# Kernel tuning notes

Measured on AMD Instinct MI355X. Metric: run time of the kernel, lower is better.

## Reference

```python
import jax, jax.numpy as jnp
import numpy as np
import math

B, S, D_MODEL, H = 2, 2048, 2048, 16
HD = D_MODEL // H  # head_dim = 128


def setup_inputs() -> dict:
    key = jax.random.key(0)
    ks = jax.random.split(key, 10)
    x = jax.random.normal(ks[0], (B, S, D_MODEL), dtype=jnp.float32)
    # RoPE tables: interleaved-pair layout matching rotate_half (adjacent dims form pairs)
    inv_freq = 1.0 / (10000.0 ** (jnp.arange(0, HD, 2, dtype=jnp.float32) / HD))  # [HD/2]
    angles = jnp.arange(S, dtype=jnp.float32)[:, None] * inv_freq[None, :]        # [S, HD/2]
    angles = jnp.repeat(angles, 2, axis=-1)                                       # [S, HD]
    cos, sin = jnp.cos(angles), jnp.sin(angles)
    # causal mask (1 = keep), broadcastable to [B,H,S,S]
    attn_mask = jnp.tril(jnp.ones((S, S), dtype=bool))[None, None]
    scale = 1.0 / math.sqrt(D_MODEL)
    Wq = jax.random.normal(ks[1], (D_MODEL, D_MODEL), dtype=jnp.float32) * scale
    Wk = jax.random.normal(ks[2], (D_MODEL, D_MODEL), dtype=jnp.float32) * scale
    Wv = jax.random.normal(ks[3], (D_MODEL, D_MODEL), dtype=jnp.float32) * scale
    Wo = jax.random.normal(ks[4], (D_MODEL, D_MODEL), dtype=jnp.float32) * scale
    bq = jnp.zeros((D_MODEL,), jnp.float32)
    bk = jnp.zeros((D_MODEL,), jnp.float32)
    bv = jnp.zeros((D_MODEL,), jnp.float32)
    bo = jnp.zeros((D_MODEL,), jnp.float32)
    return {"x": x, "cos": cos, "sin": sin, "attn_mask": attn_mask,
            "Wq": Wq, "bq": bq, "Wk": Wk, "bk": bk, "Wv": Wv, "bv": bv, "Wo": Wo, "bo": bo}


def _rotate_half(x):
    # pairs adjacent dims: (x0,x1) -> (-x1,x0)
    xr = x.reshape(*x.shape[:-1], -1, 2)
    x1, x2 = xr[..., 0], xr[..., 1]
    return jnp.stack([-x2, x1], axis=-1).reshape(x.shape)


def reference(x, cos, sin, attn_mask, Wq, bq, Wk, bk, Wv, bv, Wo, bo):
    b, s, _ = x.shape
    q = (x @ Wq.T + bq).reshape(b, s, H, HD).transpose(0, 2, 1, 3)  # [B,H,S,HD]
    k = (x @ Wk.T + bk).reshape(b, s, H, HD).transpose(0, 2, 1, 3)
    v = (x @ Wv.T + bv).reshape(b, s, H, HD).transpose(0, 2, 1, 3)
    c = cos[None, None]  # [1,1,S,HD]
    sn = sin[None, None]
    q = q * c + _rotate_half(q) * sn
    k = k * c + _rotate_half(k) * sn
    scores = jnp.einsum('bhqd,bhkd->bhqk', q, k) / math.sqrt(HD)  # [B,H,S,S]
    scores = jnp.where(attn_mask, scores, -jnp.inf)
    attn = jax.nn.softmax(scores, axis=-1)
    out = jnp.einsum('bhqk,bhkd->bhqd', attn, v)  # [B,H,S,HD]
    out = out.transpose(0, 2, 1, 3).reshape(b, s, H * HD)
    return out @ Wo.T + bo
```

## Files before the change

kernel.cpp:

```cpp
#include <hip/hip_runtime.h>
#include <math.h>

typedef __attribute__((ext_vector_type(8))) __bf16 bf16x8;
typedef __attribute__((ext_vector_type(4))) float f32x4;
typedef __attribute__((ext_vector_type(4))) unsigned short us4;
typedef unsigned short u16;
typedef unsigned int u32;

#define DEVI static __device__ __forceinline__

DEVI u16 f2bf(float f) {
  union { float f; unsigned u; } v; v.f = f;
  unsigned r = v.u + 0x7fffu + ((v.u >> 16) & 1u);
  return (u16)(r >> 16);
}

DEVI void async16(const void* g, void* l) {
  __builtin_amdgcn_global_load_lds((const __attribute__((address_space(1))) void*)g,
                                   (__attribute__((address_space(3))) void*)l, 16, 0, 0);
}

DEVI u32 pkbf(float lo, float hi) {
  u32 r;
  asm("v_cvt_pk_bf16_f32 %0, %1, %2" : "=v"(r) : "v"(lo), "v"(hi));
  return r;
}

__global__ __launch_bounds__(256)
void cast_all(const float* __restrict__ x,
              const float* __restrict__ wq, const float* __restrict__ wk,
              const float* __restrict__ wv, const float* __restrict__ wo,
              u16* __restrict__ xb, u16* __restrict__ wqb, u16* __restrict__ wkb,
              u16* __restrict__ wvb, u16* __restrict__ wob)
{
  const int NX = 4096 * 2048, NW = 2048 * 2048;
  int i = (blockIdx.x * 256 + threadIdx.x) * 4;
  const float* src; u16* dst; int off;
  if (i < NX)               { src = x;  dst = xb;  off = i; }
  else if (i < NX + NW)     { src = wq; dst = wqb; off = i - NX; }
  else if (i < NX + 2 * NW) { src = wk; dst = wkb; off = i - NX - NW; }
  else if (i < NX + 3 * NW) { src = wv; dst = wvb; off = i - NX - 2 * NW; }
  else                      { src = wo; dst = wob; off = i - NX - 3 * NW; }
  float4 v = *(const float4*)(src + off);
  us4 o = { f2bf(v.x), f2bf(v.y), f2bf(v.z), f2bf(v.w) };
  *(us4*)(dst + off) = o;
}

template<int MODE>
__global__ __launch_bounds__(256, 3)
void gemm_bt(const u16* __restrict__ A, const u16* __restrict__ B,
             const float* __restrict__ bias,
             const float* __restrict__ cosT, const float* __restrict__ sinT,
             void* __restrict__ outp)
{
  __shared__ __align__(16) u16 As[8192];
  __shared__ __align__(16) u16 Bs[8192];
  const int t = threadIdx.x, w = t >> 6, lane = t & 63;
  const int lrow = lane & 15, lk8 = (lane >> 4) * 8;
  const int brow = blockIdx.y * 128, bcol = blockIdx.x * 128;
  const int wr = (w >> 1) * 64, wc = (w & 1) * 64;

  u32 sA[4], sB[4];
#pragma unroll
  for (int r = 0; r < 4; ++r) {
    const int q = (r * 256 + t) * 16;
    const int row = q >> 7;
    const int cb = (q ^ ((row & 7) << 4)) & 127;
    sA[r] = (u32)((brow + row) * 2048 + (cb >> 1));
    sB[r] = (u32)((bcol + row) * 2048 + (cb >> 1));
  }

  int offA[4][2], offB[4][2];
#pragma unroll
  for (int m = 0; m < 4; ++m)
#pragma unroll
    for (int kk = 0; kk < 2; ++kk) {
      int row = wr + m * 16 + lrow;
      offA[m][kk] = (row * 128 + (kk * 32 + lk8) * 2) ^ ((row & 7) << 4);
      row = wc + m * 16 + lrow;
      offB[m][kk] = (row * 128 + (kk * 32 + lk8) * 2) ^ ((row & 7) << 4);
    }

  f32x4 acc[4][4] = {};

  for (int k0 = 0; k0 < 2048; k0 += 64) {
#pragma unroll
    for (int r = 0; r < 4; ++r) {
      async16(A + sA[r] + k0, (char*)As + (r * 256 + t) * 16);
      async16(B + sB[r] + k0, (char*)Bs + (r * 256 + t) * 16);
    }
    __syncthreads();
#pragma unroll
    for (int kk = 0; kk < 2; ++kk) {
      bf16x8 a[4], b[4];
#pragma unroll
      for (int m = 0; m < 4; ++m) a[m] = *(const bf16x8*)((char*)As + offA[m][kk]);
#pragma unroll
      for (int n = 0; n < 4; ++n) b[n] = *(const bf16x8*)((char*)Bs + offB[n][kk]);
#pragma unroll
      for (int m = 0; m < 4; ++m)
#pragma unroll
        for (int n = 0; n < 4; ++n)
          acc[m][n] = __builtin_amdgcn_mfma_f32_16x16x32_bf16(a[m], b[n], acc[m][n], 0, 0, 0);
    }
    __syncthreads();
  }

#pragma unroll
  for (int mi = 0; mi < 4; ++mi) {
#pragma unroll
    for (int ni = 0; ni < 4; ++ni) {
      f32x4 v = acc[mi][ni];
      const int row0 = brow + wr + mi * 16 + (lane >> 4) * 4;
      const int col = bcol + wc + ni * 16 + lrow;
      if constexpr (MODE == 3) {
        float* O = (float*)outp;
        const float bv = bias[col];
#pragma unroll
        for (int r = 0; r < 4; ++r)
          O[(size_t)(row0 + r) * 2048 + col] = v[r] + bv;
      } else if constexpr (MODE == 0 || MODE == 1) {
        u16* O = (u16*)outp;
        const float bv = bias[col];
        const int h = col >> 7, d = col & 127;
        const float sgn = (d & 1) ? 1.f : -1.f;
        const float QSCL = 0.08838834764831845f * 1.44269504088896340f;
#pragma unroll
        for (int r = 0; r < 4; ++r) {
          const int row = row0 + r, bb = row >> 11, s = row & 2047;
          float q = v[r] + bv;
          float p = __shfl_xor(q, 1);
          float o = q * cosT[s * 128 + d] + sgn * p * sinT[s * 128 + d];
          if constexpr (MODE == 0) o *= QSCL;
          u16* base = O + ((size_t)(bb * 16 + h) * 2048 + s) * 128;
          if constexpr (MODE == 0) {
            base[d] = f2bf(o);
          } else {
            *(u16*)((char*)base + (((unsigned)(d << 1)) ^ (unsigned)((s & 7) << 4))) = f2bf(o);
          }
        }
      } else {
        u16* O = (u16*)outp;
        const float bv = bias[col];
        const int h = col >> 7, d = col & 127;
        const int bb = row0 >> 11, s = row0 & 2047;
        us4 ov;
#pragma unroll
        for (int r = 0; r < 4; ++r) ov[r] = f2bf(v[r] + bv);
        const int l = s & 63;
        const int kt = l >> 4, g2 = (l >> 2) & 3;
        const int c = ((kt >> 1) << 5) + (g2 << 3) + ((kt & 1) << 2);
        u16* base = O + ((size_t)(bb * 16 + h) * 128 + d) * 2048 + (s & ~63);
        *(us4*)((char*)base + ((unsigned)(c << 1) ^ (unsigned)((d & 7) << 4))) = ov;
      }
    }
  }
}

__global__ __launch_bounds__(256, 2)
void attn_fwd(const u16* __restrict__ Q, const u16* __restrict__ K,
              const u16* __restrict__ Vt, u16* __restrict__ AO)
{
  __shared__ __align__(16) u16 Ks[2][64 * 128];
  __shared__ __align__(16) u16 Vs[2][128 * 64];
  const int t = threadIdx.x, w = t >> 6, lane = t & 63;
  const int lrow = lane & 15, g = lane >> 4, lk8 = g * 8;
  const int id = blockIdx.x;
  const int bh = (id & 7) | (((id >> 3) & 3) << 3);
  const int pr = id >> 5;
  const u16* Qg = Q + (size_t)bh * 2048 * 128;
  const u16* Kg = K + (size_t)bh * 2048 * 128;
  const u16* Vg = Vt + (size_t)bh * 128 * 2048;
  const int bb = bh >> 4, h = bh & 15;

  for (int half = 0; half < 2; ++half) {
    const int qt = half ? (31 - pr) : pr;
    const int q0 = qt * 64, qw = q0 + w * 16;
    const int nkv = qt + 1;
    const int qg = qw + lrow;

    bf16x8 qf[4];
#pragma unroll
    for (int c = 0; c < 4; ++c)
      qf[c] = *(const bf16x8*)(Qg + (size_t)(qw + lrow) * 128 + lk8 + c * 32);

    f32x4 acc_o[8] = {};
    float m = -1e30f, lsum = 0.f;

    auto stage = [&](int i, int b) {
#pragma unroll
      for (int r = 0; r < 4; ++r) {
        int e = (r * 256 + t) * 8;
        async16(Kg + (size_t)i * 8192 + e, &Ks[b][r * 2048 + w * 512]);
        async16(Vg + (size_t)(e >> 6) * 2048 + i * 64 + (e & 63), &Vs[b][r * 2048 + w * 512]);
      }
    };

    stage(0, 0);
    for (int i = 0; i < nkv; ++i) {
      const int cur = i & 1;
      const bool pfch = (i + 1) < nkv;
      if (pfch) stage(i + 1, cur ^ 1);
      if (pfch) asm volatile("s_waitcnt vmcnt(8)" ::: "memory");
      else      asm volatile("s_waitcnt vmcnt(0)" ::: "memory");
      __builtin_amdgcn_s_barrier();
      __builtin_amdgcn_sched_barrier(0);

      f32x4 sc[4];
      __builtin_amdgcn_s_setprio(1);
#pragma unroll
      for (int kt = 0; kt < 4; ++kt) {
        f32x4 s = {};
        const int krow = kt * 16 + lrow;
        const char* kbase = (const char*)(&Ks[cur][krow * 128]);
        const unsigned sw = (unsigned)((krow & 7) << 4);
#pragma unroll
        for (int c = 0; c < 4; ++c) {
          bf16x8 kf = *(const bf16x8*)(kbase + ((unsigned)((lk8 + c * 32) << 1) ^ sw));
          s = __builtin_amdgcn_mfma_f32_16x16x32_bf16(kf, qf[c], s, 0, 0, 0);
        }
        sc[kt] = s;
      }
      __builtin_amdgcn_s_setprio(0);

      float p[4][4];
      const bool lastblk = (i == qt);
      if (lastblk) {
#pragma unroll
        for (int kt = 0; kt < 4; ++kt)
#pragma unroll
          for (int r = 0; r < 4; ++r) {
            int kg = i * 64 + kt * 16 + g * 4 + r;
            p[kt][r] = (kg > qg) ? -1e30f : sc[kt][r];
          }
      } else {
#pragma unroll
        for (int kt = 0; kt < 4; ++kt)
#pragma unroll
          for (int r = 0; r < 4; ++r) p[kt][r] = sc[kt][r];
      }

      float mm = p[0][0];
#pragma unroll
      for (int kt = 0; kt < 4; ++kt)
#pragma unroll
        for (int r = 0; r < 4; ++r) mm = fmaxf(mm, p[kt][r]);
      mm = fmaxf(mm, __shfl_xor(mm, 16));
      mm = fmaxf(mm, __shfl_xor(mm, 32));

      float rs = 0.f;
      if (__any(mm > m + 8.f)) {
        const float mn = fmaxf(m, mm);
        const float corr = exp2f(m - mn);
        m = mn;
#pragma unroll
        for (int kt = 0; kt < 4; ++kt)
#pragma unroll
          for (int r = 0; r < 4; ++r) { p[kt][r] = exp2f(p[kt][r] - m); rs += p[kt][r]; }
        rs += __shfl_xor(rs, 16);
        rs += __shfl_xor(rs, 32);
        lsum = lsum * corr + rs;
#pragma unroll
        for (int nt = 0; nt < 8; ++nt)
#pragma unroll
          for (int r = 0; r < 4; ++r) acc_o[nt][r] *= corr;
      } else {
#pragma unroll
        for (int kt = 0; kt < 4; ++kt)
#pragma unroll
          for (int r = 0; r < 4; ++r) { p[kt][r] = exp2f(p[kt][r] - m); rs += p[kt][r]; }
        rs += __shfl_xor(rs, 16);
        rs += __shfl_xor(rs, 32);
        lsum += rs;
      }

      bf16x8 pb[2];
#pragma unroll
      for (int kc = 0; kc < 2; ++kc) {
        union { u32 d[4]; bf16x8 v; } u;
        u.d[0] = pkbf(p[2 * kc][0], p[2 * kc][1]);
        u.d[1] = pkbf(p[2 * kc][2], p[2 * kc][3]);
        u.d[2] = pkbf(p[2 * kc + 1][0], p[2 * kc + 1][1]);
        u.d[3] = pkbf(p[2 * kc + 1][2], p[2 * kc + 1][3]);
        pb[kc] = u.v;
      }

      __builtin_amdgcn_s_setprio(1);
#pragma unroll
      for (int nt = 0; nt < 8; ++nt) {
        const int vrow = nt * 16 + lrow;
        const char* vbase = (const char*)(&Vs[cur][vrow * 64]);
        const unsigned sw2 = (unsigned)((vrow & 7) << 4);
#pragma unroll
        for (int kc = 0; kc < 2; ++kc) {
          bf16x8 vf = *(const bf16x8*)(vbase + ((unsigned)((lk8 + kc * 32) << 1) ^ sw2));
          acc_o[nt] = __builtin_amdgcn_mfma_f32_16x16x32_bf16(vf, pb[kc], acc_o[nt], 0, 0, 0);
        }
      }
      __builtin_amdgcn_s_setprio(0);
      __builtin_amdgcn_s_barrier();
    }

    const float inv_l = 1.f / lsum;
#pragma unroll
    for (int nt = 0; nt < 8; ++nt) {
      us4 ov;
#pragma unroll
      for (int r = 0; r < 4; ++r) ov[r] = f2bf(acc_o[nt][r] * inv_l);
      *(us4*)(AO + ((size_t)(bb * 2048 + qg)) * 2048 + h * 128 + nt * 16 + g * 4) = ov;
    }
  }
}

extern "C" void kernel_launch(void* const* d_in, const int* in_sizes, int n_in,
                              void* d_out, int out_size, void* d_ws, size_t ws_size,
                              hipStream_t stream) {
  const float* x    = (const float*)d_in[0];
  const float* cosT = (const float*)d_in[1];
  const float* sinT = (const float*)d_in[2];
  const float* Wq   = (const float*)d_in[4];
  const float* bq   = (const float*)d_in[5];
  const float* Wk   = (const float*)d_in[6];
  const float* bk   = (const float*)d_in[7];
  const float* Wv   = (const float*)d_in[8];
  const float* bv   = (const float*)d_in[9];
  const float* Wo   = (const float*)d_in[10];
  const float* bo   = (const float*)d_in[11];
  float* out = (float*)d_out;

  char* ws = (char*)d_ws;
  u16* xb  = (u16*)(ws);
  u16* Wqb = (u16*)(ws + (16u << 20));
  u16* Wkb = (u16*)(ws + (24u << 20));
  u16* Wvb = (u16*)(ws + (32u << 20));
  u16* Wob = (u16*)(ws + (40u << 20));
  u16* Qb  = (u16*)(ws + (48u << 20));
  u16* Kb  = (u16*)(ws + (64u << 20));
  u16* Vtb = (u16*)(ws + (80u << 20));
  u16* AOb = (u16*)(ws + (96u << 20));

  cast_all<<<24576, 256, 0, stream>>>(x, Wq, Wk, Wv, Wo, xb, Wqb, Wkb, Wvb, Wob);

  dim3 gg(16, 32);
  gemm_bt<0><<<gg, 256, 0, stream>>>(xb, Wqb, bq, cosT, sinT, (void*)Qb);
  gemm_bt<1><<<gg, 256, 0, stream>>>(xb, Wkb, bk, cosT, sinT, (void*)Kb);
  gemm_bt<2><<<gg, 256, 0, stream>>>(xb, Wvb, bv, nullptr, nullptr, (void*)Vtb);

  attn_fwd<<<512, 256, 0, stream>>>(Qb, Kb, Vtb, AOb);

  gemm_bt<3><<<gg, 256, 0, stream>>>(AOb, Wob, bo, nullptr, nullptr, (void*)out);
}
```

Before: 247.2 us.

## Use FP8 V and probabilities for PV matmul on later query tiles

The V projection now also writes an FP8 (e4m3) transposed copy of V into the workspace slot that previously held Wq in bf16, since that buffer is dead after the Q GEMM. For query tiles at index 4 and above, the attention kernel stages the FP8 V tile (half the bytes), packs the softmax probabilities to FP8, and uses the fp8 16x16x32 MFMA for the PV product. This halves V load and LDS traffic for most tiles and lowers PV precision. The risks are accuracy loss from FP8 probabilities and V, and an extra FP8 write pass in the V GEMM epilogue.

```diff
diff --git a/kernel.cpp b/kernel.cpp
--- a/kernel.cpp
+++ b/kernel.cpp
@@ -1,4 +1,5 @@
 #include <hip/hip_runtime.h>
+#include <hip/hip_fp8.h>
 #include <math.h>
 
 typedef __attribute__((ext_vector_type(8))) __bf16 bf16x8;
@@ -6,6 +7,7 @@
 typedef __attribute__((ext_vector_type(4))) unsigned short us4;
 typedef unsigned short u16;
 typedef unsigned int u32;
+typedef unsigned char u8;
 
 #define DEVI static __device__ __forceinline__
 
@@ -13,6 +15,17 @@
   union { float f; unsigned u; } v; v.f = f;
   unsigned r = v.u + 0x7fffu + ((v.u >> 16) & 1u);
   return (u16)(r >> 16);
+}
+
+DEVI u8 f2fp8(float f) {
+  __hip_fp8_e4m3 v(f);
+  return *(u8*)&v;
+}
+
+DEVI u32 pk4fp8(float a, float b, float c, float d) {
+  int w = __builtin_amdgcn_cvt_pk_fp8_f32(a, b, 0, false);
+  w = __builtin_amdgcn_cvt_pk_fp8_f32(c, d, w, true);
+  return (u32)w;
 }
 
 DEVI void async16(const void* g, void* l) {
@@ -51,7 +64,7 @@
 void gemm_bt(const u16* __restrict__ A, const u16* __restrict__ B,
              const float* __restrict__ bias,
              const float* __restrict__ cosT, const float* __restrict__ sinT,
-             void* __restrict__ outp)
+             void* __restrict__ outp, void* __restrict__ outp2)
 {
   __shared__ __align__(16) u16 As[8192];
   __shared__ __align__(16) u16 Bs[8192];
@@ -145,13 +158,19 @@
         const int h = col >> 7, d = col & 127;
         const int bb = row0 >> 11, s = row0 & 2047;
         us4 ov;
-#pragma unroll
-        for (int r = 0; r < 4; ++r) ov[r] = f2bf(v[r] + bv);
+        float vb[4];
+#pragma unroll
+        for (int r = 0; r < 4; ++r) { vb[r] = v[r] + bv; ov[r] = f2bf(vb[r]); }
         const int l = s & 63;
         const int kt = l >> 4, g2 = (l >> 2) & 3;
         const int c = ((kt >> 1) << 5) + (g2 << 3) + ((kt & 1) << 2);
         u16* base = O + ((size_t)(bb * 16 + h) * 128 + d) * 2048 + (s & ~63);
         *(us4*)((char*)base + ((unsigned)(c << 1) ^ (unsigned)((d & 7) << 4))) = ov;
+        u8* O8 = (u8*)outp2;
+        u32 w8 = (u32)f2fp8(vb[0]) | ((u32)f2fp8(vb[1]) << 8) |
+                 ((u32)f2fp8(vb[2]) << 16) | ((u32)f2fp8(vb[3]) << 24);
+        u8* base8 = O8 + ((size_t)(bb * 16 + h) * 128 + d) * 2048 + (s & ~63);
+        *(u32*)(base8 + ((unsigned)c ^ (unsigned)((d & 7) << 3))) = w8;
       }
     }
   }
@@ -159,10 +178,11 @@
 
 __global__ __launch_bounds__(256, 2)
 void attn_fwd(const u16* __restrict__ Q, const u16* __restrict__ K,
-              const u16* __restrict__ Vt, u16* __restrict__ AO)
+              const u16* __restrict__ Vt, const u8* __restrict__ Vt8,
+              u16* __restrict__ AO)
 {
   __shared__ __align__(16) u16 Ks[2][64 * 128];
-  __shared__ __align__(16) u16 Vs[2][128 * 64];
+  __shared__ __align__(16) char Vsb[2][16384];
   const int t = threadIdx.x, w = t >> 6, lane = t & 63;
   const int lrow = lane & 15, g = lane >> 4, lk8 = g * 8;
   const int id = blockIdx.x;
@@ -171,6 +191,7 @@
   const u16* Qg = Q + (size_t)bh * 2048 * 128;
   const u16* Kg = K + (size_t)bh * 2048 * 128;
   const u16* Vg = Vt + (size_t)bh * 128 * 2048;
+  const u8*  V8g = Vt8 + (size_t)bh * 128 * 2048;
   const int bb = bh >> 4, h = bh & 15;
 
   for (int half = 0; half < 2; ++half) {
@@ -178,6 +199,7 @@
     const int q0 = qt * 64, qw = q0 + w * 16;
     const int nkv = qt + 1;
     const int qg = qw + lrow;
+    const bool f8 = (qt >= 4);
 
     bf16x8 qf[4];
 #pragma unroll
@@ -192,7 +214,21 @@
       for (int r = 0; r < 4; ++r) {
         int e = (r * 256 + t) * 8;
         async16(Kg + (size_t)i * 8192 + e, &Ks[b][r * 2048 + w * 512]);
-        async16(Vg + (size_t)(e >> 6) * 2048 + i * 64 + (e & 63), &Vs[b][r * 2048 + w * 512]);
+      }
+      if (f8) {
+#pragma unroll
+        for (int r = 0; r < 2; ++r) {
+          int e = (r * 256 + t) * 16;
+          async16(V8g + (size_t)(e >> 6) * 2048 + i * 64 + (e & 63),
+                  Vsb[b] + r * 4096 + w * 1024);
+        }
+      } else {
+#pragma unroll
+        for (int r = 0; r < 4; ++r) {
+          int e = (r * 256 + t) * 8;
+          async16(Vg + (size_t)(e >> 6) * 2048 + i * 64 + (e & 63),
+                  (u16*)Vsb[b] + r * 2048 + w * 512);
+        }
       }
     };
 
@@ -201,8 +237,12 @@
       const int cur = i & 1;
       const bool pfch = (i + 1) < nkv;
       if (pfch) stage(i + 1, cur ^ 1);
-      if (pfch) asm volatile("s_waitcnt vmcnt(8)" ::: "memory");
-      else      asm volatile("s_waitcnt vmcnt(0)" ::: "memory");
+      if (pfch) {
+        if (f8) asm volatile("s_waitcnt vmcnt(6)" ::: "memory");
+        else    asm volatile("s_waitcnt vmcnt(8)" ::: "memory");
+      } else {
+        asm volatile("s_waitcnt vmcnt(0)" ::: "memory");
+      }
       __builtin_amdgcn_s_barrier();
       __builtin_amdgcn_sched_barrier(0);
 
@@ -274,30 +314,52 @@
         lsum += rs;
       }
 
-      bf16x8 pb[2];
-#pragma unroll
-      for (int kc = 0; kc < 2; ++kc) {
-        union { u32 d[4]; bf16x8 v; } u;
-        u.d[0] = pkbf(p[2 * kc][0], p[2 * kc][1]);
-        u.d[1] = pkbf(p[2 * kc][2], p[2 * kc][3]);
-        u.d[2] = pkbf(p[2 * kc + 1][0], p[2 * kc + 1][1]);
-        u.d[3] = pkbf(p[2 * kc + 1][2], p[2 * kc + 1][3]);
-        pb[kc] = u.v;
-      }
-
-      __builtin_amdgcn_s_setprio(1);
-#pragma unroll
-      for (int nt = 0; nt < 8; ++nt) {
-        const int vrow = nt * 16 + lrow;
-        const char* vbase = (const char*)(&Vs[cur][vrow * 64]);
-        const unsigned sw2 = (unsigned)((vrow & 7) << 4);
+      if (f8) {
+        long pb8[2];
 #pragma unroll
         for (int kc = 0; kc < 2; ++kc) {
-          bf16x8 vf = *(const bf16x8*)(vbase + ((unsigned)((lk8 + kc * 32) << 1) ^ sw2));
-          acc_o[nt] = __builtin_amdgcn_mfma_f32_16x16x32_bf16(vf, pb[kc], acc_o[nt], 0, 0, 0);
-        }
-      }
-      __builtin_amdgcn_s_setprio(0);
+          union { u32 d[2]; long l; } u;
+          u.d[0] = pk4fp8(p[2 * kc][0], p[2 * kc][1], p[2 * kc][2], p[2 * kc][3]);
+          u.d[1] = pk4fp8(p[2 * kc + 1][0], p[2 * kc + 1][1], p[2 * kc + 1][2], p[2 * kc + 1][3]);
+          pb8[kc] = u.l;
+        }
+        __builtin_amdgcn_s_setprio(1);
+#pragma unroll
+        for (int nt = 0; nt < 8; ++nt) {
+          const u8* vbase = (const u8*)Vsb[cur] + (nt * 16 + lrow) * 64;
+          const unsigned sw2 = (unsigned)((lrow & 7) << 3);
+#pragma unroll
+          for (int kc = 0; kc < 2; ++kc) {
+            long vf8 = *(const long*)(vbase + ((unsigned)(kc * 32 + g * 8) ^ sw2));
+            acc_o[nt] = __builtin_amdgcn_mfma_f32_16x16x32_fp8_fp8(vf8, pb8[kc], acc_o[nt], 0, 0, 0);
+          }
+        }
+        __builtin_amdgcn_s_setprio(0);
+      } else {
+        bf16x8 pb[2];
+#pragma unroll
+        for (int kc = 0; kc < 2; ++kc) {
+          union { u32 d[4]; bf16x8 v; } u;
+          u.d[0] = pkbf(p[2 * kc][0], p[2 * kc][1]);
+          u.d[1] = pkbf(p[2 * kc][2], p[2 * kc][3]);
+          u.d[2] = pkbf(p[2 * kc + 1][0], p[2 * kc + 1][1]);
+          u.d[3] = pkbf(p[2 * kc + 1][2], p[2 * kc + 1][3]);
+          pb[kc] = u.v;
+        }
+        __builtin_amdgcn_s_setprio(1);
+#pragma unroll
+        for (int nt = 0; nt < 8; ++nt) {
+          const int vrow = nt * 16 + lrow;
+          const char* vbase = (const char*)((u16*)Vsb[cur] + vrow * 64);
+          const unsigned sw2 = (unsigned)((vrow & 7) << 4);
+#pragma unroll
+          for (int kc = 0; kc < 2; ++kc) {
+            bf16x8 vf = *(const bf16x8*)(vbase + ((unsigned)((lk8 + kc * 32) << 1) ^ sw2));
+            acc_o[nt] = __builtin_amdgcn_mfma_f32_16x16x32_bf16(vf, pb[kc], acc_o[nt], 0, 0, 0);
+          }
+        }
+        __builtin_amdgcn_s_setprio(0);
+      }
       __builtin_amdgcn_s_barrier();
     }
 
@@ -338,15 +400,16 @@
   u16* Kb  = (u16*)(ws + (64u << 20));
   u16* Vtb = (u16*)(ws + (80u << 20));
   u16* AOb = (u16*)(ws + (96u << 20));
+  u8*  Vt8 = (u8*)(ws + (16u << 20));
 
   cast_all<<<24576, 256, 0, stream>>>(x, Wq, Wk, Wv, Wo, xb, Wqb, Wkb, Wvb, Wob);
 
   dim3 gg(16, 32);
-  gemm_bt<0><<<gg, 256, 0, stream>>>(xb, Wqb, bq, cosT, sinT, (void*)Qb);
-  gemm_bt<1><<<gg, 256, 0, stream>>>(xb, Wkb, bk, cosT, sinT, (void*)Kb);
-  gemm_bt<2><<<gg, 256, 0, stream>>>(xb, Wvb, bv, nullptr, nullptr, (void*)Vtb);
-
-  attn_fwd<<<512, 256, 0, stream>>>(Qb, Kb, Vtb, AOb);
-
-  gemm_bt<3><<<gg, 256, 0, stream>>>(AOb, Wob, bo, nullptr, nullptr, (void*)out);
-}
+  gemm_bt<0><<<gg, 256, 0, stream>>>(xb, Wqb, bq, cosT, sinT, (void*)Qb, nullptr);
+  gemm_bt<1><<<gg, 256, 0, stream>>>(xb, Wkb, bk, cosT, sinT, (void*)Kb, nullptr);
+  gemm_bt<2><<<gg, 256, 0, stream>>>(xb, Wvb, bv, nullptr, nullptr, (void*)Vtb, (void*)Vt8);
+
+  attn_fwd<<<512, 256, 0, stream>>>(Qb, Kb, Vtb, Vt8, AOb);
+
+  gemm_bt<3><<<gg, 256, 0, stream>>>(AOb, Wob, bo, nullptr, nullptr, (void*)out, nullptr);
+}
```

Result: no change. 248.2 us (+0.4%).
